# Performance work log

Measured on AMD Instinct MI355X. Metric: run time of the kernel, lower is better.

The kernel has to match this reference:

```python
import jax, jax.numpy as jnp
from jax import lax
import numpy as np

N_CHARS = 256
EMB = 512
HID = 2048
T = 4096


def setup_inputs() -> dict:
    key = jax.random.key(0)
    ks = jax.random.split(key, 12)
    s = 0.02
    D = EMB + HID
    return {
        "input_seq": jax.random.randint(ks[0], (T,), 0, N_CHARS, dtype=jnp.int64)
        if jax.config.jax_enable_x64 else jax.random.randint(ks[0], (T,), 0, N_CHARS, dtype=jnp.int32),
        "hidden": jnp.zeros((HID,), jnp.float32),
        "cell": jnp.zeros((HID,), jnp.float32),
        "emb": jax.random.normal(ks[1], (N_CHARS, EMB), jnp.float32) * s,
        "Wf": jax.random.normal(ks[2], (D, HID), jnp.float32) * s,
        "bf": jnp.zeros((HID,), jnp.float32),
        "Wi": jax.random.normal(ks[3], (D, HID), jnp.float32) * s,
        "bi": jnp.zeros((HID,), jnp.float32),
        "Wo": jax.random.normal(ks[4], (D, HID), jnp.float32) * s,
        "bo": jnp.zeros((HID,), jnp.float32),
        "Wc": jax.random.normal(ks[5], (D, HID), jnp.float32) * s,
        "bc": jnp.zeros((HID,), jnp.float32),
        "Wout": jax.random.normal(ks[6], (HID, N_CHARS), jnp.float32) * s,
        "bout": jnp.zeros((N_CHARS,), jnp.float32),
    }


def reference(input_seq, hidden, cell, emb, Wf, bf, Wi, bi, Wo, bo, Wc, bc, Wout, bout):
    x = emb[input_seq]  # [T, EMB] — embed all steps up-front

    def step(carry, xt):
        h, c = carry
        comb = jnp.concatenate([xt, h])          # [EMB+HID], cat order (input, hidden)
        f = jax.nn.sigmoid(comb @ Wf + bf)
        i = jax.nn.sigmoid(comb @ Wi + bi)
        o = jax.nn.sigmoid(comb @ Wo + bo)
        g = jnp.tanh(comb @ Wc + bc)
        c_new = f * c + i * g
        h_new = o * jnp.tanh(c_new)
        return (h_new, c_new), h_new

    (h_fin, c_fin), hs = lax.scan(step, (hidden, cell), x)  # hs: [T, HID]
    out = hs @ Wout + bout  # [T, N_CHARS] — fc_output applied per step (batched here, same math)
    return out, h_fin, c_fin
```

## Files before the change

### kernel.cpp

```cpp
#include <hip/hip_runtime.h>
#include <hip/hip_bf16.h>

#define T_STEPS 4096
#define HID 2048
#define EMB 512
#define NCH 256

typedef unsigned long long u64;
typedef unsigned int u32;

__device__ __forceinline__ float sigm_f(float x) {
    x = fminf(fmaxf(x, -30.f), 30.f);
    return 1.f / (1.f + __expf(-x));
}
__device__ __forceinline__ float tanh_f(float x) {
    float ax = fminf(fabsf(x), 15.f);
    float e = __expf(2.f * ax);
    float t = (e - 1.f) / (e + 1.f);
    return copysignf(t, x);
}

__global__ __launch_bounds__(256) void a1_proj(
    const float* __restrict__ emb,
    const float* __restrict__ Wf, const float* __restrict__ bf,
    const float* __restrict__ Wi, const float* __restrict__ bi,
    const float* __restrict__ Wo, const float* __restrict__ bo,
    const float* __restrict__ Wc, const float* __restrict__ bc,
    float* __restrict__ P) {
    const int g = blockIdx.x & 3;
    const int c0 = (blockIdx.x >> 2) << 3;
    const float* W = (g == 0) ? Wf : (g == 1) ? Wi : (g == 2) ? Wo : Wc;
    const float* b = (g == 0) ? bf : (g == 1) ? bi : (g == 2) ? bo : bc;
    __shared__ float el[8][EMB];
    const int tid = threadIdx.x;
    for (int q = tid; q < 8 * EMB; q += 256)
        el[q >> 9][q & 511] = emb[(size_t)(c0 + (q >> 9)) * EMB + (q & 511)];
    __syncthreads();
    float acc[8][8];
#pragma unroll
    for (int cc = 0; cc < 8; ++cc)
#pragma unroll
        for (int k = 0; k < 8; ++k) acc[cc][k] = 0.f;
    for (int e = 0; e < EMB; ++e) {
        float w8[8];
#pragma unroll
        for (int k = 0; k < 8; ++k) w8[k] = W[(size_t)e * HID + tid + (k << 8)];
#pragma unroll
        for (int cc = 0; cc < 8; ++cc) {
            float xe = el[cc][e];
#pragma unroll
            for (int k = 0; k < 8; ++k) acc[cc][k] = fmaf(xe, w8[k], acc[cc][k]);
        }
    }
    float bb[8];
#pragma unroll
    for (int k = 0; k < 8; ++k) bb[k] = b[tid + (k << 8)];
#pragma unroll
    for (int cc = 0; cc < 8; ++cc)
#pragma unroll
        for (int k = 0; k < 8; ++k)
            P[((((size_t)(c0 + cc) << 11) + tid + (k << 8)) << 2) + g] = acc[cc][k] + bb[k];
}

__global__ void a2_transpose(const float* __restrict__ Wf, const float* __restrict__ Wi,
                             const float* __restrict__ Wo, const float* __restrict__ Wc,
                             float* __restrict__ WT) {
    __shared__ float tile[32][33];
    const int g = blockIdx.z;
    const float* W = (g == 0) ? Wf : (g == 1) ? Wi : (g == 2) ? Wo : Wc;
    const int k0 = blockIdx.x << 5, j0 = blockIdx.y << 5;
    const int tx = threadIdx.x, ty = threadIdx.y;
#pragma unroll
    for (int i = 0; i < 32; i += 8)
        tile[ty + i][tx] = W[(size_t)(EMB + k0 + ty + i) * HID + j0 + tx];
    __syncthreads();
#pragma unroll
    for (int i = 0; i < 32; i += 8)
        WT[(((size_t)g * HID + j0 + ty + i) << 11) + k0 + tx] = tile[tx][ty + i];
}

__global__ void a3_init(const float* __restrict__ hidden, u64* __restrict__ hbuf, int ring) {
    int j = blockIdx.x * 256 + threadIdx.x;
    int total = ring << 11;
    if (j < total)
        hbuf[j] = (j < HID) ? (u64)__float_as_uint(hidden[j]) : 0xFFFFFFFF00000000ull;
}

__global__ __launch_bounds__(512, 2) void b_lstm(
    const int* __restrict__ seq, const float* __restrict__ cell,
    const float* __restrict__ P, const float* __restrict__ WT,
    u64* __restrict__ hbuf, float* __restrict__ hs, float* __restrict__ dout,
    int rmask) {
    __shared__ float h_lds[HID];
    __shared__ int seq_lds[T_STEPS];
    __shared__ float h_pub[8];
    __shared__ float pad_force[16000];
    const int tid = threadIdx.x;
    const int l = tid & 63;
    const int jl = tid >> 6;
    const int jglob = (blockIdx.x << 3) + jl;

    ((volatile float*)pad_force)[tid] = 0.f;

    for (int q = tid; q < T_STEPS; q += 512) seq_lds[q] = seq[q];

    float4 wreg[4][8];
#pragma unroll
    for (int g = 0; g < 4; ++g)
#pragma unroll
        for (int q = 0; q < 8; ++q)
            wreg[g][q] = *(const float4*)&WT[(((size_t)g * HID + jglob) << 11) + (q << 8) + (l << 2)];

    float c_reg = cell[jglob];
    float h_last = 0.f;
    __syncthreads();

    for (int s = 0; s < T_STEPS; ++s) {
        if (s > 0) {
            if (tid < 8) {
                u64 pv = ((u64)(u32)s << 32) | (u64)__float_as_uint(h_pub[tid]);
                u64* dst = hbuf + ((size_t)(s & rmask) << 11) + (blockIdx.x << 3) + tid;
                asm volatile(
                    "global_store_dwordx2 %0, %1, off sc1\n\t"
                    "global_store_dwordx2 %0, %1, off sc0 sc1"
                    ::"v"(dst), "v"(pv) : "memory");
            } else if (tid < 16) {
                hs[((size_t)(s - 1) << 11) + (blockIdx.x << 3) + (tid - 8)] = h_pub[tid - 8];
            }
        }

        const int ch = seq_lds[s];
        const float4 xg = *(const float4*)(P + ((((size_t)ch << 11) + jglob) << 2));

        const u64* src = hbuf + ((size_t)(s & rmask) << 11);
        const u64* p0 = src + tid;
        const u64* p1 = p0 + 512;
        const u64* p2 = p0 + 1024;
        const u64* p3 = p0 + 1536;
        const u32 target = (u32)s;
        for (;;) {
            u64 t0, t1, t2, t3;
            asm volatile(
                "global_load_dwordx2 %0, %4, off sc0 sc1\n\t"
                "global_load_dwordx2 %1, %5, off sc0 sc1\n\t"
                "global_load_dwordx2 %2, %6, off sc0 sc1\n\t"
                "global_load_dwordx2 %3, %7, off sc0 sc1\n\t"
                "s_waitcnt vmcnt(0)"
                : "=&v"(t0), "=&v"(t1), "=&v"(t2), "=&v"(t3)
                : "v"(p0), "v"(p1), "v"(p2), "v"(p3)
                : "memory");
            u32 bad = ((u32)(t0 >> 32) ^ target) | ((u32)(t1 >> 32) ^ target) |
                      ((u32)(t2 >> 32) ^ target) | ((u32)(t3 >> 32) ^ target);
            if (bad == 0) {
                h_lds[tid]        = __uint_as_float((u32)t0);
                h_lds[512 + tid]  = __uint_as_float((u32)t1);
                h_lds[1024 + tid] = __uint_as_float((u32)t2);
                h_lds[1536 + tid] = __uint_as_float((u32)t3);
                break;
            }
        }
        __syncthreads();

        float a0 = 0.f, a1 = 0.f, a2 = 0.f, a3 = 0.f;
#pragma unroll
        for (int q = 0; q < 8; ++q) {
            const float4 hv = *(const float4*)&h_lds[(q << 8) + (l << 2)];
            a0 = fmaf(wreg[0][q].x, hv.x, a0);
            a0 = fmaf(wreg[0][q].y, hv.y, a0);
            a0 = fmaf(wreg[0][q].z, hv.z, a0);
            a0 = fmaf(wreg[0][q].w, hv.w, a0);
            a1 = fmaf(wreg[1][q].x, hv.x, a1);
            a1 = fmaf(wreg[1][q].y, hv.y, a1);
            a1 = fmaf(wreg[1][q].z, hv.z, a1);
            a1 = fmaf(wreg[1][q].w, hv.w, a1);
            a2 = fmaf(wreg[2][q].x, hv.x, a2);
            a2 = fmaf(wreg[2][q].y, hv.y, a2);
            a2 = fmaf(wreg[2][q].z, hv.z, a2);
            a2 = fmaf(wreg[2][q].w, hv.w, a2);
            a3 = fmaf(wreg[3][q].x, hv.x, a3);
            a3 = fmaf(wreg[3][q].y, hv.y, a3);
            a3 = fmaf(wreg[3][q].z, hv.z, a3);
            a3 = fmaf(wreg[3][q].w, hv.w, a3);
        }
        a0 += __shfl_xor(a0, 32, 64);
        a1 += __shfl_xor(a1, 32, 64);
        a2 += __shfl_xor(a2, 32, 64);
        a3 += __shfl_xor(a3, 32, 64);
        float u0 = (l < 32) ? a0 : a2;
        float u1 = (l < 32) ? a1 : a3;
        u0 += __shfl_xor(u0, 16, 64);
        u1 += __shfl_xor(u1, 16, 64);
        float w = ((l & 16) == 0) ? u0 : u1;
        w += __shfl_xor(w, 8, 64);
        w += __shfl_xor(w, 4, 64);
        w += __shfl_xor(w, 2, 64);
        w += __shfl_xor(w, 1, 64);
        const float sf = __shfl(w, 0, 64);
        const float si = __shfl(w, 16, 64);
        const float so = __shfl(w, 32, 64);
        const float sg = __shfl(w, 48, 64);

        const float pf = sf + xg.x, pi = si + xg.y, po = so + xg.z, pg = sg + xg.w;
        const float f = sigm_f(pf);
        const float ii = sigm_f(pi);
        const float oo = sigm_f(po);
        const float gg = tanh_f(pg);
        c_reg = fmaf(f, c_reg, ii * gg);
        h_last = oo * tanh_f(c_reg);

        if (l == 0) h_pub[jl] = h_last;
        __syncthreads();
    }
    if (tid < 8) {
        hs[((size_t)(T_STEPS - 1) << 11) + (blockIdx.x << 3) + tid] = h_pub[tid];
    }
    if (l == 0) {
        dout[(size_t)T_STEPS * NCH + jglob] = h_last;
        dout[(size_t)T_STEPS * NCH + HID + jglob] = c_reg;
    }
}

__global__ __launch_bounds__(256) void c_out(
    const float* __restrict__ hs, const float* __restrict__ Wout,
    const float* __restrict__ bout, float* __restrict__ out) {
    __shared__ float hsl[16][NCH];
    const int tid = threadIdx.x;
    const int bt = blockIdx.x << 4;
    float acc[16];
#pragma unroll
    for (int q = 0; q < 16; ++q) acc[q] = 0.f;
    for (int kc = 0; kc < 8; ++kc) {
#pragma unroll
        for (int q = 0; q < 16; ++q)
            hsl[q][tid] = hs[(((size_t)(bt + q)) << 11) + (kc << 8) + tid];
        __syncthreads();
        for (int kk = 0; kk < 256; ++kk) {
            float w = Wout[(size_t)((kc << 8) + kk) * NCH + tid];
#pragma unroll
            for (int q = 0; q < 16; ++q) acc[q] = fmaf(hsl[q][kk], w, acc[q]);
        }
        __syncthreads();
    }
    const float bb = bout[tid];
#pragma unroll
    for (int q = 0; q < 16; ++q) out[(size_t)(bt + q) * NCH + tid] = acc[q] + bb;
}

extern "C" void kernel_launch(void* const* d_in, const int* in_sizes, int n_in,
                              void* d_out, int out_size, void* d_ws, size_t ws_size,
                              hipStream_t stream) {
    const int* seq = (const int*)d_in[0];
    const float* hidden = (const float*)d_in[1];
    const float* cell = (const float*)d_in[2];
    const float* emb = (const float*)d_in[3];
    const float* Wf = (const float*)d_in[4];
    const float* bf = (const float*)d_in[5];
    const float* Wi = (const float*)d_in[6];
    const float* bi = (const float*)d_in[7];
    const float* Wo = (const float*)d_in[8];
    const float* bo = (const float*)d_in[9];
    const float* Wc = (const float*)d_in[10];
    const float* bc = (const float*)d_in[11];
    const float* Wout = (const float*)d_in[12];
    const float* bout = (const float*)d_in[13];
    float* out = (float*)d_out;

    float* wsf = (float*)d_ws;
    u64* hbuf = (u64*)d_ws;
    float* WT = wsf + 8192;
    float* P = WT + (size_t)4 * HID * HID;
    float* hs = P + (size_t)NCH * HID * 4;

    a1_proj<<<128, 256, 0, stream>>>(emb, Wf, bf, Wi, bi, Wo, bo, Wc, bc, P);
    a2_transpose<<<dim3(64, 64, 4), dim3(32, 8), 0, stream>>>(Wf, Wi, Wo, Wc, WT);
    a3_init<<<17, 256, 0, stream>>>(hidden, hbuf, 2);
    b_lstm<<<256, 512, 0, stream>>>(seq, cell, P, WT, hbuf, hs, out, 1);
    c_out<<<256, 256, 0, stream>>>(hs, Wout, bout, out);
}
```

Measured before the change: 12.39 ms.

## Replicate hidden-state exchange buffer per XCC to localize spin-polling reads

Each block now writes its new h values to eight replicas of the double-buffered exchange ring, one per XCC, using system-scope atomic stores. Readers poll only the replica indexed by their own XCC ID. The aim is to keep the spin-wait polling on data that can stay in the local XCC's L2 instead of going to coherent memory. In exchange, writes grow eightfold per step and visibility depends on system-scope atomic stores rather than the explicit sc0/sc1 cache-bypass store pair.

```diff
diff --git a/kernel.cpp b/kernel.cpp
--- a/kernel.cpp
+++ b/kernel.cpp
@@ -79,18 +79,19 @@
         WT[(((size_t)g * HID + j0 + ty + i) << 11) + k0 + tx] = tile[tx][ty + i];
 }
 
-__global__ void a3_init(const float* __restrict__ hidden, u64* __restrict__ hbuf, int ring) {
+__global__ void a3_init(const float* __restrict__ hidden, u64* __restrict__ hbuf) {
     int j = blockIdx.x * 256 + threadIdx.x;
-    int total = ring << 11;
-    if (j < total)
-        hbuf[j] = (j < HID) ? (u64)__float_as_uint(hidden[j]) : 0xFFFFFFFF00000000ull;
+    if (j < 8 * 4096) {
+        int within = j & 4095;
+        hbuf[j] = (within < 2048) ? (u64)__float_as_uint(hidden[within])
+                                  : 0xFFFFFFFF00000000ull;
+    }
 }
 
 __global__ __launch_bounds__(512, 2) void b_lstm(
     const int* __restrict__ seq, const float* __restrict__ cell,
     const float* __restrict__ P, const float* __restrict__ WT,
-    u64* __restrict__ hbuf, float* __restrict__ hs, float* __restrict__ dout,
-    int rmask) {
+    u64* __restrict__ hbuf, float* __restrict__ hs, float* __restrict__ dout) {
     __shared__ float h_lds[HID];
     __shared__ int seq_lds[T_STEPS];
     __shared__ float h_pub[8];
@@ -102,6 +103,10 @@
 
     ((volatile float*)pad_force)[tid] = 0.f;
 
+    u32 xcc;
+    asm("s_getreg_b32 %0, hwreg(HW_REG_XCC_ID)" : "=s"(xcc));
+    xcc &= 7;
+
     for (int q = tid; q < T_STEPS; q += 512) seq_lds[q] = seq[q];
 
     float4 wreg[4][8];
@@ -117,22 +122,20 @@
 
     for (int s = 0; s < T_STEPS; ++s) {
         if (s > 0) {
-            if (tid < 8) {
-                u64 pv = ((u64)(u32)s << 32) | (u64)__float_as_uint(h_pub[tid]);
-                u64* dst = hbuf + ((size_t)(s & rmask) << 11) + (blockIdx.x << 3) + tid;
-                asm volatile(
-                    "global_store_dwordx2 %0, %1, off sc1\n\t"
-                    "global_store_dwordx2 %0, %1, off sc0 sc1"
-                    ::"v"(dst), "v"(pv) : "memory");
-            } else if (tid < 16) {
-                hs[((size_t)(s - 1) << 11) + (blockIdx.x << 3) + (tid - 8)] = h_pub[tid - 8];
+            if (tid < 64) {
+                u64 pv = ((u64)(u32)s << 32) | (u64)__float_as_uint(h_pub[tid & 7]);
+                u64* dst = hbuf + ((size_t)(tid >> 3) << 12) + ((size_t)(s & 1) << 11)
+                         + (blockIdx.x << 3) + (tid & 7);
+                __hip_atomic_store(dst, pv, __ATOMIC_RELAXED, __HIP_MEMORY_SCOPE_SYSTEM);
+            } else if (tid < 72) {
+                hs[((size_t)(s - 1) << 11) + (blockIdx.x << 3) + (tid - 64)] = h_pub[tid - 64];
             }
         }
 
         const int ch = seq_lds[s];
         const float4 xg = *(const float4*)(P + ((((size_t)ch << 11) + jglob) << 2));
 
-        const u64* src = hbuf + ((size_t)(s & rmask) << 11);
+        const u64* src = hbuf + ((size_t)xcc << 12) + ((size_t)(s & 1) << 11);
         const u64* p0 = src + tid;
         const u64* p1 = p0 + 512;
         const u64* p2 = p0 + 1024;
@@ -267,13 +270,13 @@
 
     float* wsf = (float*)d_ws;
     u64* hbuf = (u64*)d_ws;
-    float* WT = wsf + 8192;
+    float* WT = wsf + 65536;
     float* P = WT + (size_t)4 * HID * HID;
     float* hs = P + (size_t)NCH * HID * 4;
 
     a1_proj<<<128, 256, 0, stream>>>(emb, Wf, bf, Wi, bi, Wo, bo, Wc, bc, P);
     a2_transpose<<<dim3(64, 64, 4), dim3(32, 8), 0, stream>>>(Wf, Wi, Wo, Wc, WT);
-    a3_init<<<17, 256, 0, stream>>>(hidden, hbuf, 2);
-    b_lstm<<<256, 512, 0, stream>>>(seq, cell, P, WT, hbuf, hs, out, 1);
+    a3_init<<<128, 256, 0, stream>>>(hidden, hbuf);
+    b_lstm<<<256, 512, 0, stream>>>(seq, cell, P, WT, hbuf, hs, out);
     c_out<<<256, 256, 0, stream>>>(hs, Wout, bout, out);
 }
```

Result: faster. 10.79 ms (-13.0%).
